# Optimization experiments

Hardware: AMD Instinct MI355X
Metric: run time of the kernel (lower is better)

## Reference

```python
import jax, jax.numpy as jnp
import numpy as np

B, N, CIN = 16, 8192, 64
S = 1024          # num_centroids
K = 32            # num_neighbours
RADIUS = 0.2
MLP = [CIN + 3, 64, 64, 128]  # use_xyz=True -> +3 input channels
EPS = 1e-5


def setup_inputs() -> dict:
    key = jax.random.key(0)
    ks = jax.random.split(key, 8)
    xyz = jax.random.uniform(ks[0], (B, 3, N), dtype=jnp.float32)   # unit cube
    feature = jax.random.normal(ks[1], (B, CIN, N), dtype=jnp.float32)
    inp = {"xyz": xyz, "feature": feature}
    for i in range(3):
        cin, cout = MLP[i], MLP[i + 1]
        inp[f"W{i}"] = jax.random.normal(ks[2 + i], (cout, cin), dtype=jnp.float32) / np.sqrt(cin).astype(np.float32)
        inp[f"gamma{i}"] = jnp.ones((cout,), jnp.float32)
        inp[f"beta{i}"] = jnp.zeros((cout,), jnp.float32)
    return inp


def _fps(pts):
    # pts: [3, N]; iterative farthest point sampling starting at index 0
    n = pts.shape[1]
    def step(carry, _):
        dist, last = carry
        p = jnp.take(pts, last, axis=1)                 # [3]
        d = jnp.sum((pts - p[:, None]) ** 2, axis=0)    # [N]
        dist = jnp.minimum(dist, d)
        return (dist, jnp.argmax(dist).astype(jnp.int32)), last
    init = (jnp.full((n,), jnp.inf, pts.dtype), jnp.int32(0))
    _, idx = jax.lax.scan(step, init, None, length=S)
    return idx                                          # [S]


def _ball_query(pts, centers):
    # pts [3,N], centers [3,S] -> first K in-radius indices, padded with first hit
    n = pts.shape[1]
    d2 = jnp.sum((centers[:, :, None] - pts[:, None, :]) ** 2, axis=0)  # [S,N]
    within = jax.lax.stop_gradient(d2) < RADIUS * RADIUS
    # score decreasing in original index among in-radius points -> top_k picks
    # the first K in-range indices in original order
    score = jnp.where(within, n - jnp.arange(n, dtype=jnp.int32), 0)
    vals, idx = jax.lax.top_k(score, K)                 # [S,K]
    first = idx[:, :1]
    return jnp.where(vals > 0, idx, first)              # [S,K]


def _gather(a, idx):
    # a [C, N], idx [...] -> a[:, idx]
    return a[:, idx]


def reference(xyz, feature, W0, gamma0, beta0, W1, gamma1, beta1, W2, gamma2, beta2):
    idx = jax.vmap(_fps)(xyz)                                   # [B,S]
    new_xyz = jax.vmap(_gather)(xyz, idx)                       # [B,3,S]
    gidx = jax.vmap(_ball_query)(xyz, new_xyz)                  # [B,S,K]
    grouped_xyz = jax.vmap(_gather)(xyz, gidx) - new_xyz[..., None]   # [B,3,S,K]
    grouped_feat = jax.vmap(_gather)(feature, gidx)             # [B,CIN,S,K]
    x = jnp.concatenate([grouped_xyz, grouped_feat], axis=1)    # [B,CIN+3,S,K]
    for W, g, b in ((W0, gamma0, beta0), (W1, gamma1, beta1), (W2, gamma2, beta2)):
        x = jnp.einsum('oc,bcsk->bosk', W, x)
        mean = x.mean(axis=(0, 2, 3), keepdims=True)            # train-mode BN
        var = x.var(axis=(0, 2, 3), keepdims=True)
        x = (x - mean) * jax.lax.rsqrt(var + EPS)
        x = x * g[None, :, None, None] + b[None, :, None, None]
        x = jax.nn.relu(x)
    new_feature = x.max(axis=3)                                 # [B,128,S]
    return new_xyz, new_feature
```

## Files before the change

kernel.cpp:

```cpp
#include <hip/hip_runtime.h>


typedef unsigned short u16;
typedef unsigned int   u32;
typedef unsigned long long u64;

#define NB    16
#define NPTS  8192
#define CINF  64
#define NS    1024
#define KK    32
#define NSAMP (NB*NS*KK)

typedef _Float16 h2v   __attribute__((ext_vector_type(2)));
typedef _Float16 f16x8 __attribute__((ext_vector_type(8)));
typedef float    f32x4 __attribute__((ext_vector_type(4)));
typedef float    f32x2 __attribute__((ext_vector_type(2)));

static __device__ __forceinline__ h2v asH2(u32 x){ union{u32 u; h2v h;} v; v.u=x; return v.h; }
static __device__ __forceinline__ u32 asU32(h2v h){ union{u32 u; h2v h;} v; v.h=h; return v.u; }
static __device__ __forceinline__ u32 packh(float lo, float hi){
  union{ _Float16 h[2]; u32 u; } v;
  v.h[0]=(_Float16)lo; v.h[1]=(_Float16)hi; return v.u;
}
static __device__ __forceinline__ u16 f16b(float z){
  union{ _Float16 h; u16 s; } v; v.h=(_Float16)z; return v.s;
}
static __device__ __forceinline__ f32x4 zero4(){ f32x4 z; z[0]=0.f;z[1]=0.f;z[2]=0.f;z[3]=0.f; return z; }
static __device__ __forceinline__ f16x8 zero8h(){
  f16x8 z;
  #pragma unroll
  for (int i=0;i<8;i++) z[i]=(_Float16)0.f;
  return z;
}

static __device__ __forceinline__ float d2_exact(float ax,float ay,float az,float bx,float by,float bz){
  float dx=__fsub_rn(ax,bx), dy=__fsub_rn(ay,by), dz=__fsub_rn(az,bz);
  return __fadd_rn(__fadd_rn(__fmul_rn(dx,dx),__fmul_rn(dy,dy)),__fmul_rn(dz,dz));
}

template<int CTRL, int RMASK>
static __device__ __forceinline__ float dppfmax1(float v){
  int o = __builtin_amdgcn_update_dpp(__float_as_int(v), __float_as_int(v),
                                      CTRL, RMASK, 0xf, false);
  return fmaxf(v, __int_as_float(o));
}
template<int CTRL, int RMASK>
static __device__ __forceinline__ float dppfmin1(float v){
  int o = __builtin_amdgcn_update_dpp(__float_as_int(v), __float_as_int(v),
                                      CTRL, RMASK, 0xf, false);
  return fminf(v, __int_as_float(o));
}
template<int CTRL, int RMASK>
static __device__ __forceinline__ u32 dppumax1(u32 v){
  u32 o = (u32)__builtin_amdgcn_update_dpp((int)v, (int)v, CTRL, RMASK, 0xf, false);
  return v > o ? v : o;
}
#define RED6MAX(v) { v=dppfmax1<0xB1,0xf>(v); v=dppfmax1<0x4E,0xf>(v); v=dppfmax1<0x141,0xf>(v); \
                     v=dppfmax1<0x140,0xf>(v); v=dppfmax1<0x142,0xa>(v); v=dppfmax1<0x143,0xc>(v); }
#define RED6MIN(v) { v=dppfmin1<0xB1,0xf>(v); v=dppfmin1<0x4E,0xf>(v); v=dppfmin1<0x141,0xf>(v); \
                     v=dppfmin1<0x140,0xf>(v); v=dppfmin1<0x142,0xa>(v); v=dppfmin1<0x143,0xc>(v); }
#define RED6UMAX(v) { v=dppumax1<0xB1,0xf>(v); v=dppumax1<0x4E,0xf>(v); v=dppumax1<0x141,0xf>(v); \
                      v=dppumax1<0x140,0xf>(v); v=dppumax1<0x142,0xa>(v); v=dppumax1<0x143,0xc>(v); }
#define RED4MAXROW(v) { v=dppfmax1<0xB1,0xf>(v); v=dppfmax1<0x4E,0xf>(v); \
                        v=dppfmax1<0x141,0xf>(v); v=dppfmax1<0x140,0xf>(v); }
#define RED4UMAXROW(v) { v=dppumax1<0xB1,0xf>(v); v=dppumax1<0x4E,0xf>(v); \
                         v=dppumax1<0x141,0xf>(v); v=dppumax1<0x140,0xf>(v); }

__global__ void prep_kernel(const float* __restrict__ W0, const float* __restrict__ W1,
                            const float* __restrict__ W2,
                            u32* __restrict__ Wf1, u32* __restrict__ Wf2, u32* __restrict__ Wf3,
                            float* __restrict__ stats)
{
  const int t = threadIdx.x;
  for (int i=t;i<768;i+=256) stats[i]=0.f;
  for (int i=t;i<2048;i+=256){
    int d=i&3, lane=(i>>2)&63, kc=(i>>8)&1, tc=i>>9;
    int row=tc*16+(lane&15), k0=kc*32+(lane>>4)*8+2*d;
    Wf1[i]=packh(W0[row*67+3+k0], W0[row*67+4+k0]);
  }
  for (int i=t;i<2048;i+=256){
    int d=i&3, lane=(i>>2)&63, kc=(i>>8)&1, tc=i>>9;
    int row=tc*16+(lane&15), k0=kc*32+(lane>>4)*8+2*d;
    Wf2[i]=packh(W1[row*64+k0], W1[row*64+k0+1]);
  }
  for (int i=t;i<4096;i+=256){
    int d=i&3, lane=(i>>2)&63, kc=(i>>8)&1, tc=i>>9;
    int row=tc*16+(lane&15), k0=kc*32+(lane>>4)*8+2*d;
    Wf3[i]=packh(W2[row*64+k0], W2[row*64+k0+1]);
  }
}

__global__ __launch_bounds__(256) void transpose_kernel(const float* __restrict__ feat,
                                                        u32* __restrict__ fT32)
{
  __shared__ u16 tile[64][65];
  const int b  = blockIdx.x >> 7;
  const int n0 = (blockIdx.x & 127) << 6;
  const int t = threadIdx.x;
  const int ln = t & 63, lc = t >> 6;
  #pragma unroll
  for (int cc=0; cc<64; cc+=4){
    const int c = cc + lc;
    tile[c][ln] = f16b(feat[((size_t)b*64 + c)*NPTS + n0 + ln]);
  }
  __syncthreads();
  #pragma unroll
  for (int i=0;i<8;i++){
    const int idx = t*8 + i;
    const int row = idx >> 5, dw = idx & 31;
    u32 pair = (u32)tile[2*dw][row] | ((u32)tile[2*dw+1][row] << 16);
    fT32[((size_t)b*NPTS + n0 + row)*32 + dw] = pair;
  }
}

__global__ __launch_bounds__(1024,1) void fps_kernel(const float* __restrict__ xyz,
    float* __restrict__ out_xyz)
{
  __shared__ float sc[1024*28];
  __shared__ u16  sidx[NPTS];
  __shared__ u32  hcnt[64], hoff[64];
  __shared__ u32  s_kv[2][16], s_ki[2][16];
  const int b = blockIdx.x, t = threadIdx.x;
  const float* xb = xyz + (size_t)b*3*NPTS;
  if (t<64) hcnt[t]=0;
  __syncthreads();
  float lx[8], ly[8], lz[8]; int lcell[8];
  #pragma unroll
  for (int i=0;i<8;i++){
    const int idx = t + 1024*i;
    float x=xb[idx], y=xb[NPTS+idx], z=xb[2*NPTS+idx];
    lx[i]=x; ly[i]=y; lz[i]=z;
    int ix=(int)(x*4.f); ix = ix<0?0:(ix>3?3:ix);
    int iy=(int)(y*4.f); iy = iy<0?0:(iy>3?3:iy);
    int iz=(int)(z*4.f); iz = iz<0?0:(iz>3?3:iz);
    int m = (ix&1)|((iy&1)<<1)|((iz&1)<<2)|((ix&2)<<2)|((iy&2)<<3)|((iz&2)<<4);
    lcell[i]=m;
    atomicAdd(&hcnt[m],1u);
  }
  __syncthreads();
  if (t==0){ u32 s=0; for (int c=0;c<64;c++){ hoff[c]=s; s+=hcnt[c]; } }
  __syncthreads();
  #pragma unroll
  for (int i=0;i<8;i++){
    u32 pos = atomicAdd(&hoff[lcell[i]],1u);
    const int rb=(int)(pos>>3)*28+(int)(pos&7);
    sc[rb]=lx[i]; sc[rb+8]=ly[i]; sc[rb+16]=lz[i];
    sidx[pos]=(u16)(t+1024*i);
  }
  __syncthreads();
  const int tb = t*28;
  const f32x4 X0=*(const f32x4*)&sc[tb],   X1=*(const f32x4*)&sc[tb+4];
  const f32x4 Y0=*(const f32x4*)&sc[tb+8], Y1=*(const f32x4*)&sc[tb+12];
  const f32x4 Z0=*(const f32x4*)&sc[tb+16],Z1=*(const f32x4*)&sc[tb+20];
  float mnx,mxx,mny,mxy,mnz,mxz;
  {
    mnx=mxx=X0[0]; mny=mxy=Y0[0]; mnz=mxz=Z0[0];
    #pragma unroll
    for (int i=0;i<4;i++){
      mnx=fminf(mnx,fminf(X0[i],X1[i])); mxx=fmaxf(mxx,fmaxf(X0[i],X1[i]));
      mny=fminf(mny,fminf(Y0[i],Y1[i])); mxy=fmaxf(mxy,fmaxf(Y0[i],Y1[i]));
      mnz=fminf(mnz,fminf(Z0[i],Z1[i])); mxz=fmaxf(mxz,fmaxf(Z0[i],Z1[i]));
    }
  }
  RED6MIN(mnx) RED6MIN(mny) RED6MIN(mnz)
  RED6MAX(mxx) RED6MAX(mxy) RED6MAX(mxz)
  const float bx0=__int_as_float(__builtin_amdgcn_readlane(__float_as_int(mnx),63));
  const float bx1=__int_as_float(__builtin_amdgcn_readlane(__float_as_int(mxx),63));
  const float by0=__int_as_float(__builtin_amdgcn_readlane(__float_as_int(mny),63));
  const float by1=__int_as_float(__builtin_amdgcn_readlane(__float_as_int(mxy),63));
  const float bz0=__int_as_float(__builtin_amdgcn_readlane(__float_as_int(mnz),63));
  const float bz1=__int_as_float(__builtin_amdgcn_readlane(__float_as_int(mxz),63));
  u32 kb[8];
  {
    uint4 sp = *(const uint4*)&sidx[8*t];
    const u32 o0=sp.x&0xffffu, o1=sp.x>>16, o2=sp.y&0xffffu, o3=sp.y>>16;
    const u32 o4=sp.z&0xffffu, o5=sp.z>>16, o6=sp.w&0xffffu, o7=sp.w>>16;
    kb[0]=((8192u-o0)<<13)|(u32)(8*t+0); kb[1]=((8192u-o1)<<13)|(u32)(8*t+1);
    kb[2]=((8192u-o2)<<13)|(u32)(8*t+2); kb[3]=((8192u-o3)<<13)|(u32)(8*t+3);
    kb[4]=((8192u-o4)<<13)|(u32)(8*t+4); kb[5]=((8192u-o5)<<13)|(u32)(8*t+5);
    kb[6]=((8192u-o6)<<13)|(u32)(8*t+6); kb[7]=((8192u-o7)<<13)|(u32)(8*t+7);
  }

  f32x2 d[4];
  #pragma unroll
  for (int i=0;i<4;i++){ d[i][0]=__builtin_inff(); d[i][1]=__builtin_inff(); }
  u32 cached_kv = 0x7f800000u;
  u32 cached_ki = 0;

  float cx = xb[0], cy = xb[NPTS], cz = xb[2*NPTS];
  float rx = 0.f, ry = 0.f, rz = 0.f;
  const int lane = t & 63, wv = t >> 6, l16 = lane & 15;
  for (int step=0; step<NS; step++){
    if (step == t){ rx = cx; ry = cy; rz = cz; }
    if (step==NS-1) break;
    const float cval = __uint_as_float(cached_kv);
    float dxm = fmaxf(fmaxf(bx0-cx, cx-bx1), 0.f);
    float dym = fmaxf(fmaxf(by0-cy, cy-by1), 0.f);
    float dzm = fmaxf(fmaxf(bz0-cz, cz-bz1), 0.f);
    float lbs = ((dxm*dxm + dym*dym) + dzm*dzm) * 0.999f;
    if (!(lbs > cval)){
      {
        #pragma clang fp contract(off)
        f32x2 cpx; cpx[0]=cx; cpx[1]=cx;
        f32x2 cpy; cpy[0]=cy; cpy[1]=cy;
        f32x2 cpz; cpz[0]=cz; cpz[1]=cz;
#define UPDP(pi, PX, PY, PZ) { \
        f32x2 dx = (PX) - cpx, dy = (PY) - cpy, dz = (PZ) - cpz; \
        f32x2 t1 = dx*dx; f32x2 t2 = dy*dy; f32x2 t3 = t1 + t2; \
        f32x2 t4 = dz*dz; f32x2 dd = t3 + t4; \
        d[pi] = __builtin_elementwise_min(dd, d[pi]); }
        UPDP(0, X0.lo, Y0.lo, Z0.lo)
        UPDP(1, X0.hi, Y0.hi, Z0.hi)
        UPDP(2, X1.lo, Y1.lo, Z1.lo)
        UPDP(3, X1.hi, Y1.hi, Z1.hi)
#undef UPDP
      }
      f32x2 m0 = __builtin_elementwise_max(d[0], d[1]);
      f32x2 m1 = __builtin_elementwise_max(d[2], d[3]);
      f32x2 m2 = __builtin_elementwise_max(m0, m1);
      float bv = fmaxf(m2[0], m2[1]);
      RED6MAX(bv)
      const float wmax = __int_as_float(__builtin_amdgcn_readlane(__float_as_int(bv), 63));
      const u32 c0 = (d[0][0]==wmax)?kb[0]:0u;
      const u32 c1 = (d[0][1]==wmax)?kb[1]:0u;
      const u32 c2 = (d[1][0]==wmax)?kb[2]:0u;
      const u32 c3 = (d[1][1]==wmax)?kb[3]:0u;
      const u32 c4 = (d[2][0]==wmax)?kb[4]:0u;
      const u32 c5 = (d[2][1]==wmax)?kb[5]:0u;
      const u32 c6 = (d[3][0]==wmax)?kb[6]:0u;
      const u32 c7 = (d[3][1]==wmax)?kb[7]:0u;
      const u32 m01 = c0>c1?c0:c1, m23 = c2>c3?c2:c3;
      const u32 m45 = c4>c5?c4:c5, m67 = c6>c7?c6:c7;
      const u32 m03 = m01>m23?m01:m23, m47 = m45>m67?m45:m67;
      u32 ki = m03>m47?m03:m47;
      RED6UMAX(ki)
      cached_kv = __float_as_uint(wmax);
      cached_ki = (u32)__builtin_amdgcn_readlane((int)ki, 63);
    }
    const int p = step&1;
    if (lane==0){ s_kv[p][wv]=cached_kv; s_ki[p][wv]=cached_ki; }
    __syncthreads();
    const u32 kv2 = s_kv[p][l16], ki2 = s_ki[p][l16];
    const float kvf = __uint_as_float(kv2);
    float kvr = kvf;
    RED4MAXROW(kvr)
    u32 mki = (kvf == kvr) ? ki2 : 0u;
    RED4UMAXROW(mki)
    const int wslot = (int)((u32)__builtin_amdgcn_readfirstlane((int)mki) & 8191u);
    const int wb2 = (wslot>>3)*28, wi = wslot&7;
    cx = sc[wb2+wi]; cy = sc[wb2+8+wi]; cz = sc[wb2+16+wi];
  }
  out_xyz[(size_t)(b*3+0)*NS + t] = rx;
  out_xyz[(size_t)(b*3+1)*NS + t] = ry;
  out_xyz[(size_t)(b*3+2)*NS + t] = rz;
}

__global__ __launch_bounds__(256) void ballq_kernel(const float* __restrict__ xyz,
    const float* __restrict__ out_xyz, u16* __restrict__ gidx)
{
  const int gid = blockIdx.x*4 + (threadIdx.x>>6);
  const int lane = threadIdx.x & 63;
  const int b = gid >> 10, s = gid & (NS-1);
  const float* xb = xyz + (size_t)b*3*NPTS;
  const float cx = out_xyz[(size_t)(b*3+0)*NS+s];
  const float cy = out_xyz[(size_t)(b*3+1)*NS+s];
  const float cz = out_xyz[(size_t)(b*3+2)*NS+s];
  u16* out = gidx + (size_t)gid*KK;
  int cnt=0, first=-1;
  for (int base=0; base<NPTS; base+=64){
    const int pidx = base + lane;
    float d2 = d2_exact(cx,cy,cz, xb[pidx], xb[NPTS+pidx], xb[2*NPTS+pidx]);
    bool within = d2 < 0.04f;
    unsigned long long m = __ballot(within);
    if (m){
      if (first<0) first = base + (__ffsll(m)-1);
      int pos = cnt + (int)__popcll(m & ((1ull<<lane)-1ull));
      if (within && pos<KK) out[pos]=(u16)pidx;
      cnt += (int)__popcll(m);
      if (cnt>=KK) break;
    }
  }
  if (first<0) first=0;
  for (int posi = cnt + lane; posi < KK; posi += 64) out[posi]=(u16)first;
}

#define MFMA16(A,B,C) __builtin_amdgcn_mfma_f32_16x16x32_f16(A,B,C,0,0,0)

template<int STAGE>
__global__ __launch_bounds__(256,2) void mlp_pass(
    const float* __restrict__ xyz, const float* __restrict__ feat,
    const float* __restrict__ out_xyz, const u16* __restrict__ gidx,
    const u16* __restrict__ fT,
    const u32* __restrict__ Wf1, const u32* __restrict__ Wf2, const u32* __restrict__ Wf3,
    const float* __restrict__ W0raw,
    const float* __restrict__ affine, float* __restrict__ stats, u32* __restrict__ outMM)
{
  constexpr int TCO = (STAGE==2)?128:64;
  __shared__ alignas(16) u32 Xs[64*48];
  __shared__ float bins[2*TCO];
  __shared__ u32 mm[(STAGE==2)? 2*4*128 : 4];

  const int t = threadIdx.x;
  const int lane = t&63, w = t>>6, n = lane&15, q = lane>>4;
  const int j = t>>2, q4 = t&3;
  const int colbase = (w*16+n)*48;
  const int u_   = blockIdx.x;
  const int slot = u_ & 7, rr = u_ >> 3;
  const int bb   = slot*2 + (rr>>7);
  const int inner= rr & 127;
  if (t < 2*TCO) bins[t]=0.f;
  __syncthreads();

  #pragma unroll 1
  for (int ch=0; ch<4; ch++){
    const int ssb = (bb*128 + inner)*256 + ch*64;
    const int ss = ssb + j;
    const int s = (ss >> 5) & (NS-1);
    const int g = ((int)gidx[ss]) & (NPTS-1);
    {
      u32* Xrow = &Xs[j*48];
      if (q4==3){
        const float* xb = xyz + (size_t)bb*3*NPTS;
        float dx=__fsub_rn(xb[g],        out_xyz[(size_t)(bb*3+0)*NS+s]);
        float dy=__fsub_rn(xb[NPTS+g],   out_xyz[(size_t)(bb*3+1)*NS+s]);
        float dz=__fsub_rn(xb[2*NPTS+g], out_xyz[(size_t)(bb*3+2)*NS+s]);
        Xrow[32]=packh(dx,dy); Xrow[33]=packh(dz,0.f);
      }
      #pragma unroll
      for (int i=34+q4;i<48;i+=4) Xrow[i]=0;
    }
    const u16* fr;
    {
      const int gl = ((int)gidx[ssb + w*16 + n]) & (NPTS-1);
      fr = fT + ((size_t)bb*NPTS + gl)*64;
    }
    f32x4 acc[4];
    #pragma unroll
    for (int tc=0;tc<4;tc++) acc[tc]=zero4();
    #pragma unroll
    for (int kc=0;kc<2;kc++){
      f16x8 Bf = *(const f16x8*)(fr + kc*32 + q*8);
      #pragma unroll
      for (int tc=0;tc<4;tc++){
        f16x8 Af = *(const f16x8*)&Wf1[((tc*2+kc)*64+lane)*4];
        acc[tc] = MFMA16(Af,Bf,acc[tc]);
      }
    }
    {
      f16x8 Bf = *(const f16x8*)&Xs[colbase + 32 + q*4];
      #pragma unroll
      for (int tc=0;tc<4;tc++){
        f16x8 Af = zero8h();
        if (q==0){
          const int row = tc*16+n;
          Af[0]=(_Float16)W0raw[row*67+0];
          Af[1]=(_Float16)W0raw[row*67+1];
          Af[2]=(_Float16)W0raw[row*67+2];
        }
        acc[tc] = MFMA16(Af,Bf,acc[tc]);
      }
    }

    if constexpr (STAGE==0){
      #pragma unroll
      for (int tc=0;tc<4;tc++){
        #pragma unroll
        for (int r=0;r<4;r++){
          float s1=acc[tc][r], s2=__fmul_rn(s1,s1);
          #pragma unroll
          for (int off=1;off<16;off<<=1){ s1+=__shfl_xor(s1,off); s2+=__shfl_xor(s2,off); }
          if (n==0){ const int c=tc*16+q*4+r;
            atomicAdd(&bins[c], s1); atomicAdd(&bins[TCO+c], s2); }
        }
      }
    } else {
      #pragma unroll
      for (int tc=0;tc<4;tc++){
        const f32x4 sc4 = *(const f32x4*)&affine[tc*16+q*4];
        const f32x4 sh4 = *(const f32x4*)&affine[128+tc*16+q*4];
        Xs[colbase + tc*8+q*2]   = packh(fmaxf(fmaf(acc[tc][0],sc4[0],sh4[0]),0.f),
                                         fmaxf(fmaf(acc[tc][1],sc4[1],sh4[1]),0.f));
        Xs[colbase + tc*8+q*2+1] = packh(fmaxf(fmaf(acc[tc][2],sc4[2],sh4[2]),0.f),
                                         fmaxf(fmaf(acc[tc][3],sc4[3],sh4[3]),0.f));
      }
      f32x4 acc2[4];
      #pragma unroll
      for (int tc=0;tc<4;tc++) acc2[tc]=zero4();
      #pragma unroll
      for (int kc=0;kc<2;kc++){
        f16x8 Bf = *(const f16x8*)&Xs[colbase + kc*16 + q*4];
        #pragma unroll
        for (int tc=0;tc<4;tc++){
          f16x8 Af = *(const f16x8*)&Wf2[((tc*2+kc)*64+lane)*4];
          acc2[tc] = MFMA16(Af,Bf,acc2[tc]);
        }
      }
      if constexpr (STAGE==1){
        #pragma unroll
        for (int tc=0;tc<4;tc++){
          #pragma unroll
          for (int r=0;r<4;r++){
            float s1=acc2[tc][r], s2=__fmul_rn(s1,s1);
            #pragma unroll
            for (int off=1;off<16;off<<=1){ s1+=__shfl_xor(s1,off); s2+=__shfl_xor(s2,off); }
            if (n==0){ const int c=tc*16+q*4+r;
              atomicAdd(&bins[c], s1); atomicAdd(&bins[TCO+c], s2); }
          }
        }
      } else {
        #pragma unroll
        for (int tc=0;tc<4;tc++){
          const f32x4 sc4 = *(const f32x4*)&affine[256+tc*16+q*4];
          const f32x4 sh4 = *(const f32x4*)&affine[256+128+tc*16+q*4];
          Xs[colbase + tc*8+q*2]   = packh(fmaxf(fmaf(acc2[tc][0],sc4[0],sh4[0]),0.f),
                                           fmaxf(fmaf(acc2[tc][1],sc4[1],sh4[1]),0.f));
          Xs[colbase + tc*8+q*2+1] = packh(fmaxf(fmaf(acc2[tc][2],sc4[2],sh4[2]),0.f),
                                           fmaxf(fmaf(acc2[tc][3],sc4[3],sh4[3]),0.f));
        }
        f32x4 acc3[8];
        #pragma unroll
        for (int tc=0;tc<8;tc++) acc3[tc]=zero4();
        #pragma unroll
        for (int kc=0;kc<2;kc++){
          f16x8 Bf = *(const f16x8*)&Xs[colbase + kc*16 + q*4];
          #pragma unroll
          for (int tc=0;tc<8;tc++){
            f16x8 Af = *(const f16x8*)&Wf3[((tc*2+kc)*64+lane)*4];
            acc3[tc] = MFMA16(Af,Bf,acc3[tc]);
          }
        }
        u32* mmb = &mm[(ch&1)*512];
        #pragma unroll
        for (int tc=0;tc<8;tc++){
          #pragma unroll
          for (int r=0;r<4;r++){
            float y=acc3[tc][r];
            float s1=y, s2=__fmul_rn(y,y);
            u32 pm = packh(y, -y);
            #pragma unroll
            for (int off=1;off<16;off<<=1){
              s1+=__shfl_xor(s1,off); s2+=__shfl_xor(s2,off);
              u32 o = (u32)__shfl_xor((int)pm,off);
              pm = asU32(__builtin_elementwise_max(asH2(pm), asH2(o)));
            }
            if (n==0){ const int c=tc*16+q*4+r;
              atomicAdd(&bins[c], s1); atomicAdd(&bins[128+c], s2);
              mmb[w*128+c]=pm; }
          }
        }
        __syncthreads();
        {
          const int c = t&127, gg = t>>7;
          u32 a = mmb[(2*gg)*128+c], b2 = mmb[(2*gg+1)*128+c];
          h2v hm = __builtin_elementwise_max(asH2(a), asH2(b2));
          const int s0 = inner*8 + ch*2 + gg;
          outMM[((size_t)bb*128+c)*NS + s0] = packh((float)hm[0], -(float)hm[1]);
        }
      }
    }
  }

  __syncthreads();
  if (t < TCO){
    atomicAdd(&stats[STAGE*256 + 2*t],   bins[t]);
    atomicAdd(&stats[STAGE*256 + 2*t+1], bins[TCO+t]);
  }
}

__global__ void finalize_kernel(const float* __restrict__ st, float* __restrict__ af,
                                const float* __restrict__ gamma, const float* __restrict__ beta, int C)
{
  int c = threadIdx.x;
  if (c < C){
    float mean = st[2*c] * (1.f/524288.f);
    float var  = fmaxf(st[2*c+1] * (1.f/524288.f) - mean*mean, 0.f);
    float rstd = 1.f / sqrtf(var + 1e-5f);
    float sc = rstd * gamma[c];
    af[c]     = sc;
    af[128+c] = beta[c] - mean*sc;
  }
}

__global__ void apply_kernel(const float* __restrict__ affine, float* __restrict__ outF)
{
  const int i = blockIdx.x*256 + threadIdx.x;
  const int c = (i >> 10) & 127;
  u32 v = ((const u32*)outF)[i];
  h2v h = asH2(v);
  float sc = affine[512+c], sh = affine[512+128+c];
  float cand = (sc > 0.f) ? (float)h[0] : (float)h[1];
  outF[i] = fmaxf(fmaf(cand, sc, sh), 0.f);
}

extern "C" void kernel_launch(void* const* d_in, const int* in_sizes, int n_in,
                              void* d_out, int out_size, void* d_ws, size_t ws_size,
                              hipStream_t stream)
{
  (void)in_sizes; (void)n_in; (void)out_size; (void)ws_size;
  const float* xyz  = (const float*)d_in[0];
  const float* feat = (const float*)d_in[1];
  const float* W0 = (const float*)d_in[2];
  const float* g0 = (const float*)d_in[3];
  const float* b0 = (const float*)d_in[4];
  const float* W1 = (const float*)d_in[5];
  const float* g1 = (const float*)d_in[6];
  const float* b1 = (const float*)d_in[7];
  const float* W2 = (const float*)d_in[8];
  const float* g2 = (const float*)d_in[9];
  const float* b2 = (const float*)d_in[10];

  char* ws = (char*)d_ws;
  u16*   fT     = (u16*)  (ws + 0);
  u16*   gidx   = (u16*)  (ws + 16777216);
  u32*   Wf1    = (u32*)  (ws + 17825792);
  u32*   Wf2    = (u32*)  (ws + 17833984);
  u32*   Wf3    = (u32*)  (ws + 17842176);
  float* stats  = (float*)(ws + 17858560);
  float* affine = (float*)(ws + 17861632);

  float* out_xyz  = (float*)d_out;
  float* out_feat = (float*)d_out + (size_t)NB*3*NS;

  prep_kernel<<<1,256,0,stream>>>(W0,W1,W2,Wf1,Wf2,Wf3,stats);
  transpose_kernel<<<2048,256,0,stream>>>(feat, (u32*)fT);
  fps_kernel<<<NB,1024,0,stream>>>(xyz, out_xyz);
  ballq_kernel<<<NB*NS/4,256,0,stream>>>(xyz, out_xyz, gidx);

  mlp_pass<0><<<NSAMP/256,256,0,stream>>>(xyz,feat,out_xyz,gidx,fT,Wf1,Wf2,Wf3,W0,affine,stats,(u32*)out_feat);
  finalize_kernel<<<1,128,0,stream>>>(stats,     affine,     g0,b0, 64);
  mlp_pass<1><<<NSAMP/256,256,0,stream>>>(xyz,feat,out_xyz,gidx,fT,Wf1,Wf2,Wf3,W0,affine,stats,(u32*)out_feat);
  finalize_kernel<<<1,128,0,stream>>>(stats+256, affine+256, g1,b1, 64);
  mlp_pass<2><<<NSAMP/256,256,0,stream>>>(xyz,feat,out_xyz,gidx,fT,Wf1,Wf2,Wf3,W0,affine,stats,(u32*)out_feat);
  finalize_kernel<<<1,128,0,stream>>>(stats+512, affine+512, g2,b2, 128);
  apply_kernel<<<(NB*128*NS)/256,256,0,stream>>>(affine, out_feat);
}
```

Measured before the change: 1.589 ms.

## Fold prep and transpose into FPS launch and shorten FPS winner broadcast

Merges the weight-packing prep kernel and the feature transpose kernel into the FPS kernel as extra blocks, so they run on idle CUs alongside the 16 long-running FPS blocks instead of as separate serial launches. In the FPS loop, each lane now loads its candidate's coordinates from LDS before the cross-wave reduction, and the winner is broadcast with readlane. This takes the dependent LDS load off the critical per-step path. Transpose blocks now use 1024 threads and the full FPS LDS allocation, which may limit how many of them can be resident per CU.

```diff
diff --git a/kernel.cpp b/kernel.cpp
--- a/kernel.cpp
+++ b/kernel.cpp
@@ -67,61 +67,57 @@
 #define RED4UMAXROW(v) { v=dppumax1<0xB1,0xf>(v); v=dppumax1<0x4E,0xf>(v); \
                          v=dppumax1<0x141,0xf>(v); v=dppumax1<0x140,0xf>(v); }
 
-__global__ void prep_kernel(const float* __restrict__ W0, const float* __restrict__ W1,
-                            const float* __restrict__ W2,
-                            u32* __restrict__ Wf1, u32* __restrict__ Wf2, u32* __restrict__ Wf3,
-                            float* __restrict__ stats)
-{
-  const int t = threadIdx.x;
-  for (int i=t;i<768;i+=256) stats[i]=0.f;
-  for (int i=t;i<2048;i+=256){
-    int d=i&3, lane=(i>>2)&63, kc=(i>>8)&1, tc=i>>9;
-    int row=tc*16+(lane&15), k0=kc*32+(lane>>4)*8+2*d;
-    Wf1[i]=packh(W0[row*67+3+k0], W0[row*67+4+k0]);
-  }
-  for (int i=t;i<2048;i+=256){
-    int d=i&3, lane=(i>>2)&63, kc=(i>>8)&1, tc=i>>9;
-    int row=tc*16+(lane&15), k0=kc*32+(lane>>4)*8+2*d;
-    Wf2[i]=packh(W1[row*64+k0], W1[row*64+k0+1]);
-  }
-  for (int i=t;i<4096;i+=256){
-    int d=i&3, lane=(i>>2)&63, kc=(i>>8)&1, tc=i>>9;
-    int row=tc*16+(lane&15), k0=kc*32+(lane>>4)*8+2*d;
-    Wf3[i]=packh(W2[row*64+k0], W2[row*64+k0+1]);
-  }
-}
-
-__global__ __launch_bounds__(256) void transpose_kernel(const float* __restrict__ feat,
-                                                        u32* __restrict__ fT32)
-{
-  __shared__ u16 tile[64][65];
-  const int b  = blockIdx.x >> 7;
-  const int n0 = (blockIdx.x & 127) << 6;
-  const int t = threadIdx.x;
-  const int ln = t & 63, lc = t >> 6;
-  #pragma unroll
-  for (int cc=0; cc<64; cc+=4){
-    const int c = cc + lc;
-    tile[c][ln] = f16b(feat[((size_t)b*64 + c)*NPTS + n0 + ln]);
-  }
-  __syncthreads();
-  #pragma unroll
-  for (int i=0;i<8;i++){
-    const int idx = t*8 + i;
-    const int row = idx >> 5, dw = idx & 31;
-    u32 pair = (u32)tile[2*dw][row] | ((u32)tile[2*dw+1][row] << 16);
-    fT32[((size_t)b*NPTS + n0 + row)*32 + dw] = pair;
-  }
-}
-
 __global__ __launch_bounds__(1024,1) void fps_kernel(const float* __restrict__ xyz,
-    float* __restrict__ out_xyz)
+    float* __restrict__ out_xyz,
+    const float* __restrict__ feat, u32* __restrict__ fT32,
+    const float* __restrict__ W0, const float* __restrict__ W1,
+    const float* __restrict__ W2,
+    u32* __restrict__ Wf1, u32* __restrict__ Wf2, u32* __restrict__ Wf3,
+    float* __restrict__ stats)
 {
   __shared__ float sc[1024*28];
   __shared__ u16  sidx[NPTS];
   __shared__ u32  hcnt[64], hoff[64];
   __shared__ u32  s_kv[2][16], s_ki[2][16];
-  const int b = blockIdx.x, t = threadIdx.x;
+  const int bid = blockIdx.x, t = threadIdx.x;
+
+  if (bid == 16){
+    for (int i=t;i<768;i+=1024) stats[i]=0.f;
+    for (int i=t;i<2048;i+=1024){
+      int d=i&3, lane=(i>>2)&63, kc=(i>>8)&1, tc=i>>9;
+      int row=tc*16+(lane&15), k0=kc*32+(lane>>4)*8+2*d;
+      Wf1[i]=packh(W0[row*67+3+k0], W0[row*67+4+k0]);
+    }
+    for (int i=t;i<2048;i+=1024){
+      int d=i&3, lane=(i>>2)&63, kc=(i>>8)&1, tc=i>>9;
+      int row=tc*16+(lane&15), k0=kc*32+(lane>>4)*8+2*d;
+      Wf2[i]=packh(W1[row*64+k0], W1[row*64+k0+1]);
+    }
+    for (int i=t;i<4096;i+=1024){
+      int d=i&3, lane=(i>>2)&63, kc=(i>>8)&1, tc=i>>9;
+      int row=tc*16+(lane&15), k0=kc*32+(lane>>4)*8+2*d;
+      Wf3[i]=packh(W2[row*64+k0], W2[row*64+k0+1]);
+    }
+    return;
+  }
+  if (bid >= 17){
+    const int tb2 = bid - 17;
+    const int b  = tb2 >> 7;
+    const int n0 = (tb2 & 127) << 6;
+    u16* tile = (u16*)sc;
+    const int ln = t & 63, lc = t >> 6;
+    for (int cc = lc; cc < 64; cc += 16)
+      tile[cc*65 + ln] = f16b(feat[((size_t)b*64 + cc)*NPTS + n0 + ln]);
+    __syncthreads();
+    for (int i = t; i < 2048; i += 1024){
+      const int row = i >> 5, dw = i & 31;
+      u32 pair = (u32)tile[2*dw*65 + row] | ((u32)tile[(2*dw+1)*65 + row] << 16);
+      fT32[((size_t)b*NPTS + n0 + row)*32 + dw] = pair;
+    }
+    return;
+  }
+
+  const int b = bid;
   const float* xb = xyz + (size_t)b*3*NPTS;
   if (t<64) hcnt[t]=0;
   __syncthreads();
@@ -242,14 +238,19 @@
     if (lane==0){ s_kv[p][wv]=cached_kv; s_ki[p][wv]=cached_ki; }
     __syncthreads();
     const u32 kv2 = s_kv[p][l16], ki2 = s_ki[p][l16];
+    const int cslot = (int)(ki2 & 8191u);
+    const int cb2 = (cslot>>3)*28, ci = cslot&7;
+    const float px = sc[cb2+ci], py = sc[cb2+8+ci], pz = sc[cb2+16+ci];
     const float kvf = __uint_as_float(kv2);
     float kvr = kvf;
     RED4MAXROW(kvr)
     u32 mki = (kvf == kvr) ? ki2 : 0u;
     RED4UMAXROW(mki)
-    const int wslot = (int)((u32)__builtin_amdgcn_readfirstlane((int)mki) & 8191u);
-    const int wb2 = (wslot>>3)*28, wi = wslot&7;
-    cx = sc[wb2+wi]; cy = sc[wb2+8+wi]; cz = sc[wb2+16+wi];
+    const u32 wk = (u32)__builtin_amdgcn_readfirstlane((int)mki);
+    const int wwv = (int)((wk & 8191u) >> 9);
+    cx = __int_as_float(__builtin_amdgcn_readlane(__float_as_int(px), wwv));
+    cy = __int_as_float(__builtin_amdgcn_readlane(__float_as_int(py), wwv));
+    cz = __int_as_float(__builtin_amdgcn_readlane(__float_as_int(pz), wwv));
   }
   out_xyz[(size_t)(b*3+0)*NS + t] = rx;
   out_xyz[(size_t)(b*3+1)*NS + t] = ry;
@@ -522,9 +523,8 @@
   float* out_xyz  = (float*)d_out;
   float* out_feat = (float*)d_out + (size_t)NB*3*NS;
 
-  prep_kernel<<<1,256,0,stream>>>(W0,W1,W2,Wf1,Wf2,Wf3,stats);
-  transpose_kernel<<<2048,256,0,stream>>>(feat, (u32*)fT);
-  fps_kernel<<<NB,1024,0,stream>>>(xyz, out_xyz);
+  fps_kernel<<<16+1+2048,1024,0,stream>>>(xyz, out_xyz, feat, (u32*)fT,
+                                          W0,W1,W2, Wf1,Wf2,Wf3, stats);
   ballq_kernel<<<NB*NS/4,256,0,stream>>>(xyz, out_xyz, gidx);
 
   mlp_pass<0><<<NSAMP/256,256,0,stream>>>(xyz,feat,out_xyz,gidx,fT,Wf1,Wf2,Wf3,W0,affine,stats,(u32*)out_feat);
```

New measurement: 1.649 ms. 3.8% more time.
